# Kernel optimization log

Hardware: AMD Instinct MI355X
Metric: run time of the kernel (lower is better)

Reference implementation:

```python
import jax, jax.numpy as jnp
import numpy as np

N_NODES = 4096
N_EDGES = 128
D_X = 128
PE_DIM = 64
NUM_WALKS = 10
WALK_LEN = 5
EMBED_ROWS = 10000
EDGE_P = 0.02
NEG_INF = -1e30


def setup_inputs() -> dict:
    key = jax.random.key(0)
    kx, kh, ke = jax.random.split(key, 3)
    x = jax.random.normal(kx, (N_NODES, D_X), dtype=jnp.float32)
    # binary hypergraph incidence matrix (float, as used by torch H @ H.T)
    incidence = (jax.random.uniform(kh, (N_NODES, N_EDGES)) < EDGE_P).astype(jnp.float32)
    embed_weight = jax.random.normal(ke, (EMBED_ROWS, PE_DIM), dtype=jnp.float32) * 0.02
    return {"x": x, "incidence": incidence, "embed_weight": embed_weight}


def _sample_walks(neighbors, num_walks, walk_length, key):
    """Vectorized random walks: [W, L] node ids and [W, L] validity mask.

    Matches the torch loop: uniform multinomial over (H@H.T>0) neighbors with
    the self-loop zeroed, terminating early when a node has no neighbors.
    """
    N = neighbors.shape[0]
    nb = jax.lax.stop_gradient(neighbors) * (1.0 - jnp.eye(N, dtype=neighbors.dtype))
    logits = jnp.where(nb > 0, 0.0, NEG_INF)  # uniform over neighbors
    row_has = nb.sum(axis=1) > 0              # probs.sum() == 0 -> break
    starts = jnp.repeat(jnp.arange(N), num_walks)  # [W]
    W = starts.shape[0]

    def step(carry, k):
        cur, alive = carry
        alive = alive & row_has[cur]
        nxt = jax.random.categorical(k, logits[cur])  # [W]
        nxt = jnp.where(alive, nxt, cur)
        return (nxt, alive), (nxt, alive)

    keys = jax.random.split(key, walk_length - 1)
    _, (steps, valid) = jax.lax.scan(step, (starts, jnp.ones((W,), bool)), keys)
    walk_nodes = jnp.concatenate([starts[None, :], steps], axis=0).T     # [W, L]
    valid = jnp.concatenate([jnp.ones((1, W), bool), valid], axis=0).T   # [W, L]
    return walk_nodes, valid


def reference(x, incidence, embed_weight):
    N = x.shape[0]
    # node_neighbors = (H @ H.T > 0).float()
    neighbors = ((incidence @ incidence.T) > 0).astype(x.dtype)  # [N, N]
    walk_nodes, valid = _sample_walks(neighbors, NUM_WALKS, WALK_LEN, jax.random.key(42))

    # mean embedding of each walk over its valid (actual) length
    lens = valid.sum(axis=1).astype(x.dtype)                 # [W], >= 1
    emb = embed_weight[walk_nodes]                           # [W, L, D]
    m = (emb * valid[..., None]).sum(axis=1) / lens[:, None]  # [W, D]

    # every (walk, position) occurrence contributes m_walk to pe[node]
    idx = jnp.where(valid, walk_nodes, 0).reshape(-1)                      # [W*L]
    contrib = jnp.where(valid[..., None], m[:, None, :], 0.0)
    contrib = contrib.reshape(-1, m.shape[-1])                             # [W*L, D]
    w = valid.astype(x.dtype).reshape(-1)
    pe_sum = jax.ops.segment_sum(contrib, idx, num_segments=N)             # [N, D]
    cnt = jax.ops.segment_sum(w, idx, num_segments=N)                      # [N]
    pe = jnp.where(cnt[:, None] > 0, pe_sum / jnp.maximum(cnt, 1.0)[:, None], 0.0)
    return jnp.concatenate([x, pe], axis=-1)
```

## Files before the change

kernel.cpp:

```cpp
#include <hip/hip_runtime.h>
#include <hip/hip_fp16.h>
#include <stdint.h>

#define N_NODES   4096
#define N_EDGES   128
#define D_X       128
#define PE_DIM    64
#define NUM_WALKS 10
#define WALK_LEN  5
#define N_WALKS_TOT (N_NODES * NUM_WALKS)
#define OUT_COLS  (D_X + PE_DIM)
#define ROW_CAP   512u
#define VCAP      512u

#define OFF_MASKS   0u
#define OFF_DEG     (OFF_MASKS + N_NODES * 16u)
#define OFF_ADJ     (OFF_DEG + N_NODES * 4u)
#define OFF_WM      (OFF_ADJ + N_NODES * ROW_CAP * 2u)
#define OFF_VCNT    (OFF_WM + N_WALKS_TOT * PE_DIM * 2u)
#define OFF_VLIST   (OFF_VCNT + N_NODES * 4u)

__device__ __forceinline__ void tf2x32(uint32_t kk0, uint32_t kk1,
                                       uint32_t x0, uint32_t x1,
                                       uint32_t& o0, uint32_t& o1) {
  const uint32_t kk2 = kk0 ^ kk1 ^ 0x1BD11BDAu;
  x0 += kk0; x1 += kk1;
  auto rnd = [&](int r) {
    x0 += x1;
    x1 = (x1 << r) | (x1 >> (32 - r));
    x1 ^= x0;
  };
  rnd(13); rnd(15); rnd(26); rnd(6);   x0 += kk1; x1 += kk2 + 1u;
  rnd(17); rnd(29); rnd(16); rnd(24);  x0 += kk2; x1 += kk0 + 2u;
  rnd(13); rnd(15); rnd(26); rnd(6);   x0 += kk0; x1 += kk1 + 3u;
  rnd(17); rnd(29); rnd(16); rnd(24);  x0 += kk1; x1 += kk2 + 4u;
  rnd(13); rnd(15); rnd(26); rnd(6);   x0 += kk2; x1 += kk0 + 5u;
  o0 = x0; o1 = x1;
}

__global__ void k_masks(const float* __restrict__ inc,
                        ulonglong2* __restrict__ masks,
                        unsigned int* __restrict__ vcnt) {
  const int wid = threadIdx.x >> 6, lane = threadIdx.x & 63;
  const int i = blockIdx.x * 4 + wid;
  const float a = inc[i * N_EDGES + lane];
  const float b = inc[i * N_EDGES + 64 + lane];
  const unsigned long long m0 = __ballot(a != 0.f);
  const unsigned long long m1 = __ballot(b != 0.f);
  if (lane == 0) {
    masks[i] = make_ulonglong2(m0, m1);
    vcnt[i] = 0u;
  }
}

__global__ void __launch_bounds__(512)
k_adj(const ulonglong2* __restrict__ masks,
      unsigned short* __restrict__ adj, unsigned int* __restrict__ deg) {
  __shared__ ulonglong2 sm[N_NODES];
  for (int k = threadIdx.x; k < N_NODES; k += 512) sm[k] = masks[k];
  __syncthreads();
  const int wid = threadIdx.x >> 6, lane = threadIdx.x & 63;
  const int i = blockIdx.x * 8 + wid;
  const ulonglong2 mi = sm[i];
  unsigned short* row = adj + (unsigned int)i * ROW_CAP;
  unsigned int base = 0;
  for (int g = 0; g < N_NODES / 64; ++g) {
    const int j = g * 64 + lane;
    const ulonglong2 mj = sm[j];
    const bool pred = (((mi.x & mj.x) | (mi.y & mj.y)) != 0ull) && (j != i);
    const unsigned long long bal = __ballot(pred);
    if (pred) {
      const unsigned int off =
          (unsigned int)__popcll(bal & ((1ull << lane) - 1ull));
      const unsigned int pos = base + off;
      if (pos < ROW_CAP) row[pos] = (unsigned short)j;
    }
    base += (unsigned int)__popcll(bal);
  }
  if (lane == 0) deg[i] = (base < ROW_CAP) ? base : ROW_CAP;
}

__global__ void __launch_bounds__(256)
k_walkmean(const unsigned int* __restrict__ deg,
           const unsigned short* __restrict__ adj,
           const float* __restrict__ embed,
           __half* __restrict__ wm,
           unsigned int* __restrict__ vcnt, unsigned short* __restrict__ vlist) {
  __shared__ uint4 srec[64];
  const int tid = threadIdx.x, wid = tid >> 6, lane = tid & 63;
  const uint32_t wbase = blockIdx.x * 64u;

  if (tid < 64) {
    const uint32_t w = wbase + (uint32_t)tid;
    uint32_t r0, r1, r2, r3;
    tf2x32(0u, 42u, w, 0u, r0, r1);
    tf2x32(0u, 42u, w, 1u, r2, r3);
    const uint32_t n0 = w / NUM_WALKS;
    uint32_t n1, n2, n3, n4, nv;
    const unsigned int d0 = deg[n0];
    if (d0 == 0) {
      n1 = n2 = n3 = n4 = n0;
      nv = 1u;
    } else {
      uint32_t cur = n0;
      unsigned int d;
      cur = adj[(cur << 9) + (uint32_t)(((uint64_t)r0 * d0) >> 32)]; n1 = cur;
      d = deg[cur];
      cur = adj[(cur << 9) + (uint32_t)(((uint64_t)r1 * d) >> 32)]; n2 = cur;
      d = deg[cur];
      cur = adj[(cur << 9) + (uint32_t)(((uint64_t)r2 * d) >> 32)]; n3 = cur;
      d = deg[cur];
      cur = adj[(cur << 9) + (uint32_t)(((uint64_t)r3 * d) >> 32)]; n4 = cur;
      nv = 5u;
    }
    uint4 rec;
    rec.x = n0 | (n1 << 16);
    rec.y = n2 | (n3 << 16);
    rec.z = n4 | (nv << 16);
    rec.w = 0u;
    srec[tid] = rec;

    unsigned int s0 = atomicAdd(&vcnt[n0], 1u);
    if (s0 < VCAP) vlist[n0 * VCAP + s0] = (unsigned short)w;
    if (nv == 5u) {
      unsigned int s1 = atomicAdd(&vcnt[n1], 1u);
      if (s1 < VCAP) vlist[n1 * VCAP + s1] = (unsigned short)w;
      unsigned int s2 = atomicAdd(&vcnt[n2], 1u);
      if (s2 < VCAP) vlist[n2 * VCAP + s2] = (unsigned short)w;
      unsigned int s3 = atomicAdd(&vcnt[n3], 1u);
      if (s3 < VCAP) vlist[n3 * VCAP + s3] = (unsigned short)w;
      unsigned int s4 = atomicAdd(&vcnt[n4], 1u);
      if (s4 < VCAP) vlist[n4 * VCAP + s4] = (unsigned short)w;
    }
  }
  __syncthreads();

#pragma unroll 4
  for (int k = 0; k < 16; ++k) {
    const int widx = wid * 16 + k;
    const uint4 rc = srec[widx];
    const uint32_t a0 = rc.x & 0xFFFFu, a1 = rc.x >> 16;
    const uint32_t a2 = rc.y & 0xFFFFu, a3 = rc.y >> 16;
    const uint32_t a4 = rc.z & 0xFFFFu, anv = rc.z >> 16;
    float s = embed[a0 * PE_DIM + lane];
    if (anv == 5u) {
      s += embed[a1 * PE_DIM + lane];
      s += embed[a2 * PE_DIM + lane];
      s += embed[a3 * PE_DIM + lane];
      s += embed[a4 * PE_DIM + lane];
    }
    wm[(size_t)(wbase + widx) * PE_DIM + lane] = __float2half(s / (float)anv);
  }
}

__global__ void __launch_bounds__(256)
k_gather(const __half* __restrict__ walk_m,
         const unsigned int* __restrict__ vcnt,
         const unsigned short* __restrict__ vlist,
         const float* __restrict__ x,
         float* __restrict__ out) {
  __shared__ float red[4][PE_DIM];
  const int wid = threadIdx.x >> 6, lane = threadIdx.x & 63;
  const int v = blockIdx.x;

  if (wid == 3) {
    const float2 xv = ((const float2*)(x + (size_t)v * D_X))[lane];
    ((float2*)(out + (size_t)v * OUT_COLS))[lane] = xv;
  }

  unsigned int c = vcnt[v];
  if (c > VCAP) c = VCAP;
  const unsigned short* vl = vlist + (unsigned int)v * VCAP;

  float s = 0.f;
  for (unsigned int base = (unsigned int)wid * 8u; base < c; base += 32u) {
#pragma unroll
    for (int q = 0; q < 8; ++q) {
      const unsigned int idx = base + (unsigned int)q;
      const bool ok = idx < c;
      const unsigned int ww = ok ? (unsigned int)vl[idx] : (unsigned int)vl[0];
      const float val = __half2float(walk_m[(size_t)ww * PE_DIM + lane]);
      s += ok ? val : 0.f;
    }
  }
  red[wid][lane] = s;
  __syncthreads();
  if (wid == 0) {
    const float t = red[0][lane] + red[1][lane] + red[2][lane] + red[3][lane];
    out[(size_t)v * OUT_COLS + D_X + lane] = c ? t / (float)c : 0.f;
  }
}

extern "C" void kernel_launch(void* const* d_in, const int* in_sizes, int n_in,
                              void* d_out, int out_size, void* d_ws, size_t ws_size,
                              hipStream_t stream) {
  const float* x   = (const float*)d_in[0];
  const float* inc = (const float*)d_in[1];
  const float* emb = (const float*)d_in[2];
  float* out = (float*)d_out;

  char* ws = (char*)d_ws;
  ulonglong2*     masks = (ulonglong2*)(ws + OFF_MASKS);
  unsigned int*   deg   = (unsigned int*)(ws + OFF_DEG);
  unsigned short* adj   = (unsigned short*)(ws + OFF_ADJ);
  __half*         wm    = (__half*)(ws + OFF_WM);
  unsigned int*   vcnt  = (unsigned int*)(ws + OFF_VCNT);
  unsigned short* vlist = (unsigned short*)(ws + OFF_VLIST);

  k_masks   <<<N_NODES / 4, 256, 0, stream>>>(inc, masks, vcnt);
  k_adj     <<<N_NODES / 8, 512, 0, stream>>>(masks, adj, deg);
  k_walkmean<<<N_WALKS_TOT / 64, 256, 0, stream>>>(deg, adj, emb, wm, vcnt,
                                                   vlist);
  k_gather  <<<N_NODES, 256, 0, stream>>>(wm, vcnt, vlist, x, out);
}
```

Before: 66.87 us.

## Fuse four kernels into one cooperative persistent kernel with grid barriers

Combines the mask, adjacency, walk-mean and gather kernels into a single cooperative kernel of 512 blocks that separates the phases with custom atomic-counter grid barriers. Each block handles 8 nodes and 80 walks, and each wave does the gather for a node by itself rather than splitting it across four waves. The aim is to remove launch overhead and inter-kernel gaps. In exchange there are spin-wait barriers and less parallelism in the adjacency and gather phases, since there are fewer blocks and threads per node.

```diff
diff --git a/kernel.cpp b/kernel.cpp
--- a/kernel.cpp
+++ b/kernel.cpp
@@ -7,18 +7,41 @@
 #define D_X       128
 #define PE_DIM    64
 #define NUM_WALKS 10
-#define WALK_LEN  5
 #define N_WALKS_TOT (N_NODES * NUM_WALKS)
 #define OUT_COLS  (D_X + PE_DIM)
 #define ROW_CAP   512u
 #define VCAP      512u
+#define NBLK      512
+#define NTHR      256
+#define WPB       80
 
 #define OFF_MASKS   0u
 #define OFF_DEG     (OFF_MASKS + N_NODES * 16u)
 #define OFF_ADJ     (OFF_DEG + N_NODES * 4u)
 #define OFF_WM      (OFF_ADJ + N_NODES * ROW_CAP * 2u)
-#define OFF_VCNT    (OFF_WM + N_WALKS_TOT * PE_DIM * 2u)
+#define OFF_VCNT    (OFF_WM + (size_t)N_WALKS_TOT * PE_DIM * 2u)
 #define OFF_VLIST   (OFF_VCNT + N_NODES * 4u)
+
+__device__ unsigned int g_ctr[3];
+__device__ unsigned int g_flag[3];
+
+__device__ __forceinline__ void gbar(int i) {
+  __syncthreads();
+  if (threadIdx.x == 0) {
+    __threadfence();
+    const unsigned int t = atomicAdd(&g_ctr[i], 1u) + 1u;
+    const unsigned int target = ((t + NBLK - 1u) / NBLK) * NBLK;
+    if (t == target) {
+      atomicMax(&g_flag[i], target);
+    } else {
+      while (__hip_atomic_load(&g_flag[i], __ATOMIC_RELAXED,
+                               __HIP_MEMORY_SCOPE_AGENT) < target)
+        __builtin_amdgcn_s_sleep(1);
+    }
+    __threadfence();
+  }
+  __syncthreads();
+}
 
 __device__ __forceinline__ void tf2x32(uint32_t kk0, uint32_t kk1,
                                        uint32_t x0, uint32_t x1,
@@ -38,59 +61,61 @@
   o0 = x0; o1 = x1;
 }
 
-__global__ void k_masks(const float* __restrict__ inc,
-                        ulonglong2* __restrict__ masks,
-                        unsigned int* __restrict__ vcnt) {
-  const int wid = threadIdx.x >> 6, lane = threadIdx.x & 63;
-  const int i = blockIdx.x * 4 + wid;
-  const float a = inc[i * N_EDGES + lane];
-  const float b = inc[i * N_EDGES + 64 + lane];
-  const unsigned long long m0 = __ballot(a != 0.f);
-  const unsigned long long m1 = __ballot(b != 0.f);
-  if (lane == 0) {
-    masks[i] = make_ulonglong2(m0, m1);
-    vcnt[i] = 0u;
-  }
-}
-
-__global__ void __launch_bounds__(512)
-k_adj(const ulonglong2* __restrict__ masks,
-      unsigned short* __restrict__ adj, unsigned int* __restrict__ deg) {
+__global__ void __launch_bounds__(NTHR)
+k_mega(const float* __restrict__ x, const float* __restrict__ inc,
+       const float* __restrict__ embed, float* __restrict__ out,
+       char* __restrict__ ws) {
   __shared__ ulonglong2 sm[N_NODES];
-  for (int k = threadIdx.x; k < N_NODES; k += 512) sm[k] = masks[k];
-  __syncthreads();
-  const int wid = threadIdx.x >> 6, lane = threadIdx.x & 63;
-  const int i = blockIdx.x * 8 + wid;
-  const ulonglong2 mi = sm[i];
-  unsigned short* row = adj + (unsigned int)i * ROW_CAP;
-  unsigned int base = 0;
-  for (int g = 0; g < N_NODES / 64; ++g) {
-    const int j = g * 64 + lane;
-    const ulonglong2 mj = sm[j];
-    const bool pred = (((mi.x & mj.x) | (mi.y & mj.y)) != 0ull) && (j != i);
-    const unsigned long long bal = __ballot(pred);
-    if (pred) {
-      const unsigned int off =
-          (unsigned int)__popcll(bal & ((1ull << lane) - 1ull));
-      const unsigned int pos = base + off;
-      if (pos < ROW_CAP) row[pos] = (unsigned short)j;
-    }
-    base += (unsigned int)__popcll(bal);
-  }
-  if (lane == 0) deg[i] = (base < ROW_CAP) ? base : ROW_CAP;
-}
-
-__global__ void __launch_bounds__(256)
-k_walkmean(const unsigned int* __restrict__ deg,
-           const unsigned short* __restrict__ adj,
-           const float* __restrict__ embed,
-           __half* __restrict__ wm,
-           unsigned int* __restrict__ vcnt, unsigned short* __restrict__ vlist) {
-  __shared__ uint4 srec[64];
+  ulonglong2*     masks = (ulonglong2*)(ws + OFF_MASKS);
+  unsigned int*   deg   = (unsigned int*)(ws + OFF_DEG);
+  unsigned short* adj   = (unsigned short*)(ws + OFF_ADJ);
+  __half*         wm    = (__half*)(ws + OFF_WM);
+  unsigned int*   vcnt  = (unsigned int*)(ws + OFF_VCNT);
+  unsigned short* vlist = (unsigned short*)(ws + OFF_VLIST);
+
   const int tid = threadIdx.x, wid = tid >> 6, lane = tid & 63;
-  const uint32_t wbase = blockIdx.x * 64u;
-
-  if (tid < 64) {
+  const int blk = blockIdx.x;
+
+  if (tid < 8) vcnt[blk * 8 + tid] = 0u;
+#pragma unroll
+  for (int r = 0; r < 2; ++r) {
+    const int i = blk * 8 + wid * 2 + r;
+    const float a = inc[i * N_EDGES + lane];
+    const float b = inc[i * N_EDGES + 64 + lane];
+    const unsigned long long m0 = __ballot(a != 0.f);
+    const unsigned long long m1 = __ballot(b != 0.f);
+    if (lane == 0) masks[i] = make_ulonglong2(m0, m1);
+  }
+  gbar(0);
+
+  for (int k = tid; k < N_NODES; k += NTHR) sm[k] = masks[k];
+  __syncthreads();
+#pragma unroll
+  for (int r = 0; r < 2; ++r) {
+    const int i = blk * 8 + wid * 2 + r;
+    const ulonglong2 mi = sm[i];
+    unsigned short* row = adj + (unsigned int)i * ROW_CAP;
+    unsigned int base = 0;
+    for (int g = 0; g < N_NODES / 64; ++g) {
+      const int j = g * 64 + lane;
+      const ulonglong2 mj = sm[j];
+      const bool pred = (((mi.x & mj.x) | (mi.y & mj.y)) != 0ull) && (j != i);
+      const unsigned long long bal = __ballot(pred);
+      if (pred) {
+        const unsigned int off =
+            (unsigned int)__popcll(bal & ((1ull << lane) - 1ull));
+        const unsigned int pos = base + off;
+        if (pos < ROW_CAP) row[pos] = (unsigned short)j;
+      }
+      base += (unsigned int)__popcll(bal);
+    }
+    if (lane == 0) deg[i] = (base < ROW_CAP) ? base : ROW_CAP;
+  }
+  gbar(1);
+
+  uint4* srec = (uint4*)sm;
+  const uint32_t wbase = (uint32_t)blk * WPB;
+  if (tid < WPB) {
     const uint32_t w = wbase + (uint32_t)tid;
     uint32_t r0, r1, r2, r3;
     tf2x32(0u, 42u, w, 0u, r0, r1);
@@ -134,10 +159,9 @@
     }
   }
   __syncthreads();
-
 #pragma unroll 4
-  for (int k = 0; k < 16; ++k) {
-    const int widx = wid * 16 + k;
+  for (int k = 0; k < WPB / 4; ++k) {
+    const int widx = wid * (WPB / 4) + k;
     const uint4 rc = srec[widx];
     const uint32_t a0 = rc.x & 0xFFFFu, a1 = rc.x >> 16;
     const uint32_t a2 = rc.y & 0xFFFFu, a3 = rc.y >> 16;
@@ -151,43 +175,29 @@
     }
     wm[(size_t)(wbase + widx) * PE_DIM + lane] = __float2half(s / (float)anv);
   }
-}
-
-__global__ void __launch_bounds__(256)
-k_gather(const __half* __restrict__ walk_m,
-         const unsigned int* __restrict__ vcnt,
-         const unsigned short* __restrict__ vlist,
-         const float* __restrict__ x,
-         float* __restrict__ out) {
-  __shared__ float red[4][PE_DIM];
-  const int wid = threadIdx.x >> 6, lane = threadIdx.x & 63;
-  const int v = blockIdx.x;
-
-  if (wid == 3) {
+  gbar(2);
+
+#pragma unroll
+  for (int r = 0; r < 2; ++r) {
+    const int v = blk * 8 + wid * 2 + r;
     const float2 xv = ((const float2*)(x + (size_t)v * D_X))[lane];
     ((float2*)(out + (size_t)v * OUT_COLS))[lane] = xv;
-  }
-
-  unsigned int c = vcnt[v];
-  if (c > VCAP) c = VCAP;
-  const unsigned short* vl = vlist + (unsigned int)v * VCAP;
-
-  float s = 0.f;
-  for (unsigned int base = (unsigned int)wid * 8u; base < c; base += 32u) {
-#pragma unroll
-    for (int q = 0; q < 8; ++q) {
-      const unsigned int idx = base + (unsigned int)q;
-      const bool ok = idx < c;
-      const unsigned int ww = ok ? (unsigned int)vl[idx] : (unsigned int)vl[0];
-      const float val = __half2float(walk_m[(size_t)ww * PE_DIM + lane]);
-      s += ok ? val : 0.f;
-    }
-  }
-  red[wid][lane] = s;
-  __syncthreads();
-  if (wid == 0) {
-    const float t = red[0][lane] + red[1][lane] + red[2][lane] + red[3][lane];
-    out[(size_t)v * OUT_COLS + D_X + lane] = c ? t / (float)c : 0.f;
+
+    unsigned int c = atomicAdd(&vcnt[v], 0u);
+    if (c > VCAP) c = VCAP;
+    const unsigned short* vl = vlist + (unsigned int)v * VCAP;
+    float s = 0.f;
+    for (unsigned int b2 = 0; b2 < c; b2 += 8) {
+#pragma unroll
+      for (int q = 0; q < 8; ++q) {
+        const unsigned int idx = b2 + (unsigned int)q;
+        const bool ok = idx < c;
+        const unsigned int wwk = ok ? (unsigned int)vl[idx] : (unsigned int)vl[0];
+        const float val = __half2float(wm[(size_t)wwk * PE_DIM + lane]);
+        s += ok ? val : 0.f;
+      }
+    }
+    out[(size_t)v * OUT_COLS + D_X + lane] = c ? s / (float)c : 0.f;
   }
 }
 
@@ -198,18 +208,9 @@
   const float* inc = (const float*)d_in[1];
   const float* emb = (const float*)d_in[2];
   float* out = (float*)d_out;
-
   char* ws = (char*)d_ws;
-  ulonglong2*     masks = (ulonglong2*)(ws + OFF_MASKS);
-  unsigned int*   deg   = (unsigned int*)(ws + OFF_DEG);
-  unsigned short* adj   = (unsigned short*)(ws + OFF_ADJ);
-  __half*         wm    = (__half*)(ws + OFF_WM);
-  unsigned int*   vcnt  = (unsigned int*)(ws + OFF_VCNT);
-  unsigned short* vlist = (unsigned short*)(ws + OFF_VLIST);
-
-  k_masks   <<<N_NODES / 4, 256, 0, stream>>>(inc, masks, vcnt);
-  k_adj     <<<N_NODES / 8, 512, 0, stream>>>(masks, adj, deg);
-  k_walkmean<<<N_WALKS_TOT / 64, 256, 0, stream>>>(deg, adj, emb, wm, vcnt,
-                                                   vlist);
-  k_gather  <<<N_NODES, 256, 0, stream>>>(wm, vcnt, vlist, x, out);
-}
+
+  void* args[] = {(void*)&x, (void*)&inc, (void*)&emb, (void*)&out, (void*)&ws};
+  hipLaunchCooperativeKernel((const void*)k_mega, dim3(NBLK), dim3(NTHR),
+                             args, 0, stream);
+}
```

Result: slower. 187.0 us (+179.7%).

## Replace dense adjacency build with edge-membership lists and rejection-sampled walks

Applied to the files above, without the earlier changes.

Drops the O(N^2) k_adj kernel that built per-node neighbor lists. It instead records, per hyperedge, the member nodes in global lists via atomics during mask construction. Each walk step then samples uniformly among neighbors: it picks an edge-member slot weighted by edge size, then accepts the candidate with probability 1/k, where k is the number of shared edges. This removes a kernel launch and a large adjacency write, in exchange for serial per-thread loops with up to 16 Threefry draws per step and more divergence. It also changes the random stream, so sampled walks differ from the old kernel's. Walks per block rise from 64 to 80.

```diff
diff --git a/kernel.cpp b/kernel.cpp
--- a/kernel.cpp
+++ b/kernel.cpp
@@ -7,18 +7,19 @@
 #define D_X       128
 #define PE_DIM    64
 #define NUM_WALKS 10
-#define WALK_LEN  5
 #define N_WALKS_TOT (N_NODES * NUM_WALKS)
 #define OUT_COLS  (D_X + PE_DIM)
-#define ROW_CAP   512u
 #define VCAP      512u
+#define EMCAP     256
+#define WPB       80
 
 #define OFF_MASKS   0u
-#define OFF_DEG     (OFF_MASKS + N_NODES * 16u)
-#define OFF_ADJ     (OFF_DEG + N_NODES * 4u)
-#define OFF_WM      (OFF_ADJ + N_NODES * ROW_CAP * 2u)
-#define OFF_VCNT    (OFF_WM + N_WALKS_TOT * PE_DIM * 2u)
+#define OFF_WM      (OFF_MASKS + N_NODES * 16u)
+#define OFF_VCNT    (OFF_WM + (size_t)N_WALKS_TOT * PE_DIM * 2u)
 #define OFF_VLIST   (OFF_VCNT + N_NODES * 4u)
+
+__device__ unsigned int   g_ecnt[N_EDGES];
+__device__ unsigned short g_emem[N_EDGES * EMCAP];
 
 __device__ __forceinline__ void tf2x32(uint32_t kk0, uint32_t kk1,
                                        uint32_t x0, uint32_t x1,
@@ -38,7 +39,7 @@
   o0 = x0; o1 = x1;
 }
 
-__global__ void k_masks(const float* __restrict__ inc,
+__global__ void k_build(const float* __restrict__ inc,
                         ulonglong2* __restrict__ masks,
                         unsigned int* __restrict__ vcnt) {
   const int wid = threadIdx.x >> 6, lane = threadIdx.x & 63;
@@ -51,93 +52,123 @@
     masks[i] = make_ulonglong2(m0, m1);
     vcnt[i] = 0u;
   }
-}
-
-__global__ void __launch_bounds__(512)
-k_adj(const ulonglong2* __restrict__ masks,
-      unsigned short* __restrict__ adj, unsigned int* __restrict__ deg) {
-  __shared__ ulonglong2 sm[N_NODES];
-  for (int k = threadIdx.x; k < N_NODES; k += 512) sm[k] = masks[k];
-  __syncthreads();
-  const int wid = threadIdx.x >> 6, lane = threadIdx.x & 63;
-  const int i = blockIdx.x * 8 + wid;
-  const ulonglong2 mi = sm[i];
-  unsigned short* row = adj + (unsigned int)i * ROW_CAP;
-  unsigned int base = 0;
-  for (int g = 0; g < N_NODES / 64; ++g) {
-    const int j = g * 64 + lane;
-    const ulonglong2 mj = sm[j];
-    const bool pred = (((mi.x & mj.x) | (mi.y & mj.y)) != 0ull) && (j != i);
-    const unsigned long long bal = __ballot(pred);
-    if (pred) {
-      const unsigned int off =
-          (unsigned int)__popcll(bal & ((1ull << lane) - 1ull));
-      const unsigned int pos = base + off;
-      if (pos < ROW_CAP) row[pos] = (unsigned short)j;
-    }
-    base += (unsigned int)__popcll(bal);
-  }
-  if (lane == 0) deg[i] = (base < ROW_CAP) ? base : ROW_CAP;
+  if (a != 0.f) {
+    const unsigned int s = atomicAdd(&g_ecnt[lane], 1u);
+    if (s < EMCAP) g_emem[(lane << 8) + s] = (unsigned short)i;
+  }
+  if (b != 0.f) {
+    const unsigned int s = atomicAdd(&g_ecnt[64 + lane], 1u);
+    if (s < EMCAP) g_emem[((64 + lane) << 8) + s] = (unsigned short)i;
+  }
 }
 
 __global__ void __launch_bounds__(256)
-k_walkmean(const unsigned int* __restrict__ deg,
-           const unsigned short* __restrict__ adj,
+k_walkmean(const ulonglong2* __restrict__ masks,
            const float* __restrict__ embed,
            __half* __restrict__ wm,
            unsigned int* __restrict__ vcnt, unsigned short* __restrict__ vlist) {
-  __shared__ uint4 srec[64];
+  __shared__ uint4 srec[WPB];
+  __shared__ unsigned int secnt[N_EDGES];
   const int tid = threadIdx.x, wid = tid >> 6, lane = tid & 63;
-  const uint32_t wbase = blockIdx.x * 64u;
-
-  if (tid < 64) {
+  const uint32_t wbase = (uint32_t)blockIdx.x * WPB;
+
+  if (tid < N_EDGES) secnt[tid] = g_ecnt[tid];
+  __syncthreads();
+
+  if (tid < WPB) {
     const uint32_t w = wbase + (uint32_t)tid;
-    uint32_t r0, r1, r2, r3;
-    tf2x32(0u, 42u, w, 0u, r0, r1);
-    tf2x32(0u, 42u, w, 1u, r2, r3);
     const uint32_t n0 = w / NUM_WALKS;
-    uint32_t n1, n2, n3, n4, nv;
-    const unsigned int d0 = deg[n0];
-    if (d0 == 0) {
-      n1 = n2 = n3 = n4 = n0;
-      nv = 1u;
+    ulonglong2 cmk = masks[n0];
+
+    bool alive = false;
+    {
+      unsigned long long lo = cmk.x, hi = cmk.y;
+      while (lo) { const int e = __ffsll(lo) - 1; lo &= lo - 1;
+                   alive |= secnt[e] >= 2u; }
+      while (hi) { const int e = __ffsll(hi) - 1; hi &= hi - 1;
+                   alive |= secnt[64 + e] >= 2u; }
+    }
+
+    uint32_t nn[5];
+    nn[0] = n0;
+    uint32_t nv = 1u;
+    if (!alive) {
+      nn[1] = nn[2] = nn[3] = nn[4] = n0;
     } else {
       uint32_t cur = n0;
-      unsigned int d;
-      cur = adj[(cur << 9) + (uint32_t)(((uint64_t)r0 * d0) >> 32)]; n1 = cur;
-      d = deg[cur];
-      cur = adj[(cur << 9) + (uint32_t)(((uint64_t)r1 * d) >> 32)]; n2 = cur;
-      d = deg[cur];
-      cur = adj[(cur << 9) + (uint32_t)(((uint64_t)r2 * d) >> 32)]; n3 = cur;
-      d = deg[cur];
-      cur = adj[(cur << 9) + (uint32_t)(((uint64_t)r3 * d) >> 32)]; n4 = cur;
       nv = 5u;
-    }
+#pragma unroll
+      for (int step = 0; step < 4; ++step) {
+        uint32_t W = 0;
+        {
+          unsigned long long lo = cmk.x, hi = cmk.y;
+          while (lo) { const int e = __ffsll(lo) - 1; lo &= lo - 1;
+                       W += secnt[e]; }
+          while (hi) { const int e = __ffsll(hi) - 1; hi &= hi - 1;
+                       W += secnt[64 + e]; }
+        }
+        uint32_t nxt = cur;
+        ulonglong2 nmk = cmk;
+#pragma unroll 1
+        for (int t = 0; t < 16; ++t) {
+          uint32_t r0, r1;
+          tf2x32(0u, 42u, w, 2u + ((uint32_t)step << 4) + (uint32_t)t, r0, r1);
+          uint32_t rem = (uint32_t)(((uint64_t)r0 * W) >> 32);
+          int edge = -1;
+          {
+            unsigned long long lo = cmk.x;
+            while (lo) { const int e = __ffsll(lo) - 1; lo &= lo - 1;
+                         const uint32_t c = secnt[e];
+                         if (rem < c) { edge = e; break; }
+                         rem -= c; }
+            if (edge < 0) {
+              unsigned long long hi = cmk.y;
+              while (hi) { const int e = __ffsll(hi) - 1; hi &= hi - 1;
+                           const uint32_t c = secnt[64 + e];
+                           if (rem < c) { edge = 64 + e; break; }
+                           rem -= c; }
+            }
+          }
+          if (rem >= (uint32_t)EMCAP) continue;
+          const uint32_t cand = g_emem[(edge << 8) + rem];
+          if (cand == cur) continue;
+          const ulonglong2 km = masks[cand];
+          const uint32_t k = (uint32_t)(__popcll(km.x & cmk.x) +
+                                        __popcll(km.y & cmk.y));
+          if (k == 1u || (uint32_t)(((uint64_t)r1 * k) >> 32) == 0u) {
+            nxt = cand; nmk = km; break;
+          }
+        }
+        cur = nxt; cmk = nmk;
+        nn[step + 1] = cur;
+      }
+    }
+
     uint4 rec;
-    rec.x = n0 | (n1 << 16);
-    rec.y = n2 | (n3 << 16);
-    rec.z = n4 | (nv << 16);
+    rec.x = nn[0] | (nn[1] << 16);
+    rec.y = nn[2] | (nn[3] << 16);
+    rec.z = nn[4] | (nv << 16);
     rec.w = 0u;
     srec[tid] = rec;
 
-    unsigned int s0 = atomicAdd(&vcnt[n0], 1u);
-    if (s0 < VCAP) vlist[n0 * VCAP + s0] = (unsigned short)w;
+    unsigned int s0 = atomicAdd(&vcnt[nn[0]], 1u);
+    if (s0 < VCAP) vlist[nn[0] * VCAP + s0] = (unsigned short)w;
     if (nv == 5u) {
-      unsigned int s1 = atomicAdd(&vcnt[n1], 1u);
-      if (s1 < VCAP) vlist[n1 * VCAP + s1] = (unsigned short)w;
-      unsigned int s2 = atomicAdd(&vcnt[n2], 1u);
-      if (s2 < VCAP) vlist[n2 * VCAP + s2] = (unsigned short)w;
-      unsigned int s3 = atomicAdd(&vcnt[n3], 1u);
-      if (s3 < VCAP) vlist[n3 * VCAP + s3] = (unsigned short)w;
-      unsigned int s4 = atomicAdd(&vcnt[n4], 1u);
-      if (s4 < VCAP) vlist[n4 * VCAP + s4] = (unsigned short)w;
+      unsigned int s1 = atomicAdd(&vcnt[nn[1]], 1u);
+      if (s1 < VCAP) vlist[nn[1] * VCAP + s1] = (unsigned short)w;
+      unsigned int s2 = atomicAdd(&vcnt[nn[2]], 1u);
+      if (s2 < VCAP) vlist[nn[2] * VCAP + s2] = (unsigned short)w;
+      unsigned int s3 = atomicAdd(&vcnt[nn[3]], 1u);
+      if (s3 < VCAP) vlist[nn[3] * VCAP + s3] = (unsigned short)w;
+      unsigned int s4 = atomicAdd(&vcnt[nn[4]], 1u);
+      if (s4 < VCAP) vlist[nn[4] * VCAP + s4] = (unsigned short)w;
     }
   }
   __syncthreads();
 
 #pragma unroll 4
-  for (int k = 0; k < 16; ++k) {
-    const int widx = wid * 16 + k;
+  for (int k = 0; k < WPB / 4; ++k) {
+    const int widx = wid * (WPB / 4) + k;
     const uint4 rc = srec[widx];
     const uint32_t a0 = rc.x & 0xFFFFu, a1 = rc.x >> 16;
     const uint32_t a2 = rc.y & 0xFFFFu, a3 = rc.y >> 16;
@@ -163,6 +194,8 @@
   const int wid = threadIdx.x >> 6, lane = threadIdx.x & 63;
   const int v = blockIdx.x;
 
+  if (v == 0 && threadIdx.x < N_EDGES) g_ecnt[threadIdx.x] = 0u;
+
   if (wid == 3) {
     const float2 xv = ((const float2*)(x + (size_t)v * D_X))[lane];
     ((float2*)(out + (size_t)v * OUT_COLS))[lane] = xv;
@@ -201,15 +234,12 @@
 
   char* ws = (char*)d_ws;
   ulonglong2*     masks = (ulonglong2*)(ws + OFF_MASKS);
-  unsigned int*   deg   = (unsigned int*)(ws + OFF_DEG);
-  unsigned short* adj   = (unsigned short*)(ws + OFF_ADJ);
   __half*         wm    = (__half*)(ws + OFF_WM);
   unsigned int*   vcnt  = (unsigned int*)(ws + OFF_VCNT);
   unsigned short* vlist = (unsigned short*)(ws + OFF_VLIST);
 
-  k_masks   <<<N_NODES / 4, 256, 0, stream>>>(inc, masks, vcnt);
-  k_adj     <<<N_NODES / 8, 512, 0, stream>>>(masks, adj, deg);
-  k_walkmean<<<N_WALKS_TOT / 64, 256, 0, stream>>>(deg, adj, emb, wm, vcnt,
-                                                   vlist);
+  k_build   <<<N_NODES / 4, 256, 0, stream>>>(inc, masks, vcnt);
+  k_walkmean<<<N_WALKS_TOT / WPB, 256, 0, stream>>>(masks, emb, wm, vcnt,
+                                                    vlist);
   k_gather  <<<N_NODES, 256, 0, stream>>>(wm, vcnt, vlist, x, out);
 }
```

Result: slower. 83.87 us (+25.4%).
